# Kernel tuning notes

Hardware: AMD Instinct MI355X
Metric: run time of the kernel (lower is better)

Reference implementation:

```python
import math
import jax, jax.numpy as jnp
import numpy as np


def setup_inputs() -> dict:
    key = jax.random.key(0)
    k0, k1, k2 = jax.random.split(key, 3)
    b, c, h, w = 4, 256, 64, 64
    x = jax.random.normal(k0, (b, c, h, w), dtype=jnp.float32)
    # 1x1 conv weights stored as [out_ch, in_ch]
    qkv_w = jax.random.normal(k1, (3 * c, c), dtype=jnp.float32) / math.sqrt(c)
    qkv_b = jnp.zeros((3 * c,), dtype=jnp.float32)
    out_w = jax.random.normal(k2, (c, c), dtype=jnp.float32) / math.sqrt(c)
    out_b = jnp.zeros((c,), dtype=jnp.float32)
    return {"x": x, "qkv_w": qkv_w, "qkv_b": qkv_b, "out_w": out_w, "out_b": out_b}


def reference(x, qkv_w, qkv_b, out_w, out_b):
    b, c, h, w = x.shape
    n = h * w
    # 1x1 conv QKV projection: [b, 3c, h, w]
    qkv = jnp.einsum('oc,bchw->bohw', qkv_w, x) + qkv_b[None, :, None, None]
    # chunk along channels into q, k, v each [b, c, n]
    qkv = qkv.reshape(b, 3, c, n)
    q, k, v = qkv[:, 0], qkv[:, 1], qkv[:, 2]
    # attn[b, i, j] = sum_c k[b,c,i] * q[b,c,j] / sqrt(c); softmax over key axis (dim=-2 -> axis=1)
    scores = jnp.einsum('bcn,bcm->bnm', k, q) / math.sqrt(c)
    attn = jax.nn.softmax(scores, axis=1)
    # out[b, c, j] = sum_i v[b,c,i] * attn[b,i,j]
    o = jnp.einsum('bcn,bnm->bcm', v, attn).reshape(b, c, h, w)
    # output 1x1 conv
    return jnp.einsum('oc,bchw->bohw', out_w, o) + out_b[None, :, None, None]
```

## Files before the change

kernel.cpp:

```cpp
#include <hip/hip_runtime.h>
#include <hip/hip_bf16.h>

typedef unsigned short u16;
typedef unsigned int u32;
typedef __attribute__((ext_vector_type(8))) short short8;
typedef __attribute__((ext_vector_type(4))) short short4v;
typedef __attribute__((ext_vector_type(16))) float f32x16;
typedef __attribute__((ext_vector_type(4))) float f32x4;

#define MFMA32 __builtin_amdgcn_mfma_f32_32x32x16_bf16
#define MFMA16 __builtin_amdgcn_mfma_f32_16x16x32_bf16

#define NSEQ 4096
#define CD 256
#define CF 0.09016844005556021f

__device__ __forceinline__ u16 f2bf(float f) {
  u32 u = __float_as_uint(f);
  u += 0x7fffu + ((u >> 16) & 1u);
  return (u16)(u >> 16);
}
__device__ __forceinline__ float bf2f(short s) {
  return __uint_as_float(((u32)(u16)s) << 16);
}
__device__ __forceinline__ u32 pk2bf(float a, float b) {
  union {
    __hip_bfloat162 h;
    u32 u;
  } cv;
  cv.h = __float22bfloat162_rn(make_float2(a, b));
  return cv.u;
}
__device__ __forceinline__ void async16(const void* g, void* l) {
  __builtin_amdgcn_global_load_lds(
      (const __attribute__((address_space(1))) u32*)g,
      (__attribute__((address_space(3))) u32*)l, 16, 0, 0);
}

__global__ __launch_bounds__(256) void xpose_cast(const float* __restrict__ x,
                                                  u16* __restrict__ x_t,
                                                  const float* __restrict__ qkv_w,
                                                  const float* __restrict__ out_w,
                                                  u16* __restrict__ wq,
                                                  u16* __restrict__ wo) {
  __shared__ float tile[64][65];
  const int t = threadIdx.x;
  {
    int lin = blockIdx.x + 64 * (blockIdx.y + 4 * blockIdx.z);
    int widx = lin * 256 + t;
    if (widx < 768 * CD)
      wq[widx] = f2bf(qkv_w[widx]);
    else
      wo[widx - 768 * CD] = f2bf(out_w[widx - 768 * CD]);
  }
  const int b = blockIdx.z;
  const int n0 = blockIdx.x * 64, c0 = blockIdx.y * 64;
  const float* xb = x + (size_t)b * CD * NSEQ;
  const int cr = t >> 4, nc4 = (t & 15) * 4;
#pragma unroll
  for (int i = 0; i < 4; ++i) {
    int c = cr + 16 * i;
    float4 v = *(const float4*)(xb + (size_t)(c0 + c) * NSEQ + n0 + nc4);
    tile[c][nc4 + 0] = v.x;
    tile[c][nc4 + 1] = v.y;
    tile[c][nc4 + 2] = v.z;
    tile[c][nc4 + 3] = v.w;
  }
  __syncthreads();
  const int n = t & 63, cc = (t >> 6) * 16;
  u16* dst = x_t + (size_t)b * NSEQ * CD + (size_t)(n0 + n) * CD + c0 + cc;
#pragma unroll
  for (int j = 0; j < 4; ++j) {
    short4v pv;
#pragma unroll
    for (int r = 0; r < 4; ++r) pv[r] = (short)f2bf(tile[cc + 4 * j + r][n]);
    *(short4v*)(dst + 4 * j) = pv;
  }
}

__global__ __launch_bounds__(512, 1) void qkv_gemm3(
    const u16* __restrict__ wq, const float* __restrict__ qkv_b,
    const u16* __restrict__ x_t, u16* __restrict__ q_t, u16* __restrict__ k_t,
    u16* __restrict__ v_) {
  __shared__ u16 __align__(16) Wls[128 * 256];
  __shared__ u16 __align__(16) Bls[128 * 256];
  const int t = threadIdx.x, w = t >> 6, lane = t & 63;
  const int l31 = lane & 31, l5 = lane >> 5;
  const int os = w & 3, nh = w >> 2;
  const int n0 = blockIdx.x * 128, o0 = blockIdx.y * 128, b = blockIdx.z;
  const u16* Xb = x_t + (size_t)b * NSEQ * CD;
#pragma unroll
  for (int j = 0; j < 8; ++j) {
    int r = w * 16 + j * 2 + l5;
    async16(wq + (size_t)(o0 + r) * CD + ((l31 ^ (r & 7)) * 8),
            Wls + (w * 16 + j * 2) * 256);
    async16(Xb + (size_t)(n0 + r) * CD + ((l31 ^ (r & 7)) * 8),
            Bls + (w * 16 + j * 2) * 256);
  }
  __builtin_amdgcn_s_waitcnt(0);
  __syncthreads();
  f32x16 acc0, acc1;
#pragma unroll
  for (int i = 0; i < 16; ++i) {
    acc0[i] = 0.f;
    acc1[i] = 0.f;
  }
  const int ra = os * 32 + l31;
  const int rb0 = nh * 64 + l31, rb1 = rb0 + 32;
#pragma unroll
  for (int kc = 0; kc < 16; ++kc) {
    short8 a = *(const short8*)(Wls + ra * 256 + (((kc * 2 + l5) ^ (ra & 7)) * 8));
    short8 b0 = *(const short8*)(Bls + rb0 * 256 + (((kc * 2 + l5) ^ (rb0 & 7)) * 8));
    short8 b1 = *(const short8*)(Bls + rb1 * 256 + (((kc * 2 + l5) ^ (rb1 & 7)) * 8));
    acc0 = MFMA32(a, b0, acc0, 0, 0, 0);
    acc1 = MFMA32(a, b1, acc1, 0, 0, 0);
  }
  const int otype = blockIdx.y >> 1;
  const int obase = o0 + os * 32;
#pragma unroll
  for (int na = 0; na < 2; ++na) {
    f32x16& acc = na ? acc1 : acc0;
    const int n_g = n0 + nh * 64 + na * 32 + l31;
    if (otype < 2) {
      u16* dst = (otype == 0 ? q_t : k_t) + (size_t)b * NSEQ * CD +
                 (size_t)n_g * CD + (obase - otype * 256);
#pragma unroll
      for (int g = 0; g < 4; ++g) {
        float4 bv = *(const float4*)(qkv_b + obase + g * 8 + l5 * 4);
        const float* bp = (const float*)&bv;
        short4v pk;
#pragma unroll
        for (int r = 0; r < 4; ++r) pk[r] = (short)f2bf(acc[g * 4 + r] + bp[r]);
        *(short4v*)(dst + g * 8 + l5 * 4) = pk;
      }
    } else {
      u16* dst = v_ + (size_t)b * CD * NSEQ;
#pragma unroll
      for (int g = 0; g < 4; ++g) {
        float4 bv = *(const float4*)(qkv_b + obase + g * 8 + l5 * 4);
        const float* bp = (const float*)&bv;
#pragma unroll
        for (int r = 0; r < 4; ++r) {
          int c = obase - 512 + g * 8 + l5 * 4 + r;
          dst[(size_t)c * NSEQ + n_g] = f2bf(acc[g * 4 + r] + bp[r]);
        }
      }
    }
  }
}

__global__ __launch_bounds__(512, 4) void flash9(const u16* __restrict__ q_t,
                                                 const u16* __restrict__ k_t,
                                                 const u16* __restrict__ v_,
                                                 u16* __restrict__ opart,
                                                 float2* __restrict__ ml) {
  __shared__ u16 __align__(16) Kls[2][32 * 256];
  __shared__ u16 __align__(16) Vls[2][128 * 64];

  const int t = threadIdx.x, w = t >> 6, lane = t & 63;
  const int l31 = lane & 31, l5 = lane >> 5;
  const int l15 = lane & 15, g = lane >> 4;

  const int linear = blockIdx.x;
  const int xcd = linear & 7, slot = linear >> 3;
  const int b = xcd >> 1;
  const int q = (xcd & 1) * 2 + (slot >> 5);
  const int mblk = slot & 31;
  const int m0 = mblk * 128;
  const int nbase = q * 1024;

  const u16* Qb = q_t + (size_t)b * NSEQ * CD;
  const u16* Kb = k_t + (size_t)b * NSEQ * CD;
  const u16* Vb = v_ + (size_t)b * CD * NSEQ;

  const int mrow = m0 + w * 16 + l15;

  short8 qf[8];
#pragma unroll
  for (int kk = 0; kk < 8; ++kk)
    qf[kk] = *(const short8*)(Qb + (size_t)mrow * CD + kk * 32 + g * 8);

  const u16* ksrc[2];
#pragma unroll
  for (int j = 0; j < 2; ++j) {
    int kr = w * 4 + j * 2 + l5;
    ksrc[j] = Kb + (size_t)kr * CD + ((l31 ^ (kr & 7)) * 8);
  }
  const u16* vsrc[2];
#pragma unroll
  for (int j = 0; j < 2; ++j) {
    int c2 = w * 16 + j * 8 + (lane >> 3);
    int chl = (lane & 7) ^ (c2 & 7);
    int c = (c2 << 1) | (chl >> 2);
    vsrc[j] = Vb + (size_t)c * NSEQ + (chl & 3) * 8;
  }

#pragma unroll
  for (int j = 0; j < 2; ++j) {
    async16(ksrc[j] + (size_t)nbase * CD, &Kls[0][(w * 4 + j * 2) * 256]);
    async16(vsrc[j] + nbase, &Vls[0][(w * 16 + j * 8) * 64]);
  }

  float mst = -3.0e38f, lst = 0.f;
  f32x4 oa[16];
#pragma unroll
  for (int i = 0; i < 16; ++i)
#pragma unroll
    for (int r = 0; r < 4; ++r) oa[i][r] = 0.f;

  const int vbase =
      (l15 >> 1) * 64 + (((((l15 & 1) << 2) | g) ^ ((l15 >> 1) & 7)) * 8);
  const int kx = l15 & 7;

  for (int tt = 0; tt < 32; ++tt) {
    const int cur = tt & 1;
    __builtin_amdgcn_s_waitcnt(0);
    __syncthreads();
    if (tt + 1 < 32) {
      const int n0 = nbase + (tt + 1) * 32;
      const int nxt = cur ^ 1;
#pragma unroll
      for (int j = 0; j < 2; ++j) {
        async16(ksrc[j] + (size_t)n0 * CD, &Kls[nxt][(w * 4 + j * 2) * 256]);
        async16(vsrc[j] + n0, &Vls[nxt][(w * 16 + j * 8) * 64]);
      }
    }
    f32x4 sa0, sa1;
#pragma unroll
    for (int r = 0; r < 4; ++r) {
      sa0[r] = 0.f;
      sa1[r] = 0.f;
    }
    __builtin_amdgcn_s_setprio(1);
#pragma unroll
    for (int kk = 0; kk < 8; ++kk) {
      const int ch = kk * 4 + g;
      short8 a0 = *(const short8*)(&Kls[cur][l15 * 256 + ((ch ^ kx) * 8)]);
      short8 a1 =
          *(const short8*)(&Kls[cur][(16 + l15) * 256 + ((ch ^ kx) * 8)]);
      sa0 = MFMA16(a0, qf[kk], sa0, 0, 0, 0);
      sa1 = MFMA16(a1, qf[kk], sa1, 0, 0, 0);
    }
    __builtin_amdgcn_s_setprio(0);
    float rm = fmaxf(fmaxf(fmaxf(sa0[0], sa0[1]), fmaxf(sa0[2], sa0[3])),
                     fmaxf(fmaxf(sa1[0], sa1[1]), fmaxf(sa1[2], sa1[3])));
    rm = fmaxf(rm, __shfl_xor(rm, 16));
    rm = fmaxf(rm, __shfl_xor(rm, 32));
    float mnew = fmaxf(mst, rm * CF);
    float al = exp2f(mst - mnew);
    mst = mnew;
    float p00 = exp2f(sa0[0] * CF - mnew), p01 = exp2f(sa0[1] * CF - mnew);
    float p02 = exp2f(sa0[2] * CF - mnew), p03 = exp2f(sa0[3] * CF - mnew);
    float p10 = exp2f(sa1[0] * CF - mnew), p11 = exp2f(sa1[1] * CF - mnew);
    float p12 = exp2f(sa1[2] * CF - mnew), p13 = exp2f(sa1[3] * CF - mnew);
    float ls = ((p00 + p01) + (p02 + p03)) + ((p10 + p11) + (p12 + p13));
    ls += __shfl_xor(ls, 16);
    ls += __shfl_xor(ls, 32);
    lst = lst * al + ls;
    if (__ballot(al != 1.0f)) {
#pragma unroll
      for (int i = 0; i < 16; ++i)
#pragma unroll
        for (int r = 0; r < 4; ++r) oa[i][r] *= al;
    }
    u32 A0 = pk2bf(p00, p01), A1 = pk2bf(p02, p03);
    u32 B0 = pk2bf(p10, p11), B1 = pk2bf(p12, p13);
    const int g0 = g & 1, h = g >> 1;
    u32 ea0 = (u32)__shfl_xor((int)A0, 16), ea1 = (u32)__shfl_xor((int)A1, 16);
    u32 eb0 = (u32)__shfl_xor((int)B0, 16), eb1 = (u32)__shfl_xor((int)B1, 16);
    u32 CA0 = g0 ? ea0 : A0, CA1 = g0 ? ea1 : A1;
    u32 CA2 = g0 ? A0 : ea0, CA3 = g0 ? A1 : ea1;
    u32 CB0 = g0 ? eb0 : B0, CB1 = g0 ? eb1 : B1;
    u32 CB2 = g0 ? B0 : eb0, CB3 = g0 ? B1 : eb1;
    u32 s0 = h ? CA0 : CB0, s1 = h ? CA1 : CB1;
    u32 s2 = h ? CA2 : CB2, s3 = h ? CA3 : CB3;
    u32 r0 = (u32)__shfl_xor((int)s0, 32), r1 = (u32)__shfl_xor((int)s1, 32);
    u32 r2 = (u32)__shfl_xor((int)s2, 32), r3 = (u32)__shfl_xor((int)s3, 32);
    u32 k0 = h ? CB0 : CA0, k1 = h ? CB1 : CA1;
    u32 k2 = h ? CB2 : CA2, k3 = h ? CB3 : CA3;
    const bool own = (g0 == h);
    union {
      u32 u[4];
      short8 s8;
    } pfv;
    pfv.u[0] = own ? k0 : r0;
    pfv.u[1] = own ? k1 : r1;
    pfv.u[2] = own ? k2 : r2;
    pfv.u[3] = own ? k3 : r3;
    short8 pf = pfv.s8;
    __builtin_amdgcn_s_setprio(1);
#pragma unroll
    for (int ct = 0; ct < 16; ++ct) {
      short8 vf = *(const short8*)(&Vls[cur][ct * 512 + vbase]);
      oa[ct] = MFMA16(vf, pf, oa[ct], 0, 0, 0);
    }
    __builtin_amdgcn_s_setprio(0);
  }

  float inv = 1.0f / lst;
  u16* dst = opart + ((size_t)(q * 4 + b) * NSEQ + mrow) * CD;
#pragma unroll
  for (int ct = 0; ct < 16; ++ct) {
    short4v pk;
#pragma unroll
    for (int r = 0; r < 4; ++r) pk[r] = (short)f2bf(oa[ct][r] * inv);
    *(short4v*)(dst + ct * 16 + g * 4) = pk;
  }
  if (lane < 16)
    ml[(size_t)(q * 4 + b) * NSEQ + mrow] = make_float2(mst, lst);
}

__global__ __launch_bounds__(512, 1) void out_gemm6(
    const u16* __restrict__ wo, const float* __restrict__ out_b,
    const u16* __restrict__ opart, const float2* __restrict__ ml,
    float* __restrict__ out) {
  __shared__ u16 __align__(16) Wls[128 * 256];
  __shared__ u16 __align__(16) Bls[128 * 256];
  const int t = threadIdx.x, w = t >> 6, lane = t & 63;
  const int l31 = lane & 31, l5 = lane >> 5;
  const int os = w & 3, nh = w >> 2;
  const int n0 = blockIdx.x * 128, o0 = blockIdx.y * 128, b = blockIdx.z;
#pragma unroll
  for (int j = 0; j < 8; ++j) {
    int r = w * 16 + j * 2 + l5;
    async16(wo + (size_t)(o0 + r) * CD + ((l31 ^ (r & 7)) * 8),
            Wls + (w * 16 + j * 2) * 256);
  }
#pragma unroll
  for (int i = 0; i < 8; ++i) {
    int idx = i * 512 + t;
    int r = idx >> 5, p = idx & 31;
    int n = n0 + r;
    float2 st[4];
#pragma unroll
    for (int qq = 0; qq < 4; ++qq) st[qq] = ml[(size_t)(qq * 4 + b) * NSEQ + n];
    float M = fmaxf(fmaxf(st[0].x, st[1].x), fmaxf(st[2].x, st[3].x));
    float wt[4], tot = 0.f;
#pragma unroll
    for (int qq = 0; qq < 4; ++qq) {
      wt[qq] = st[qq].y * exp2f(st[qq].x - M);
      tot += wt[qq];
    }
    float inv = 1.0f / tot;
    float acc[8] = {};
#pragma unroll
    for (int qq = 0; qq < 4; ++qq) {
      float wq_ = wt[qq] * inv;
      short8 xq =
          *(const short8*)(opart + ((size_t)(qq * 4 + b) * NSEQ + n) * CD + p * 8);
#pragma unroll
      for (int e = 0; e < 8; ++e) acc[e] += wq_ * bf2f(xq[e]);
    }
    short8 om;
#pragma unroll
    for (int e = 0; e < 8; ++e) om[e] = (short)f2bf(acc[e]);
    *(short8*)(Bls + r * 256 + ((p ^ (r & 7)) * 8)) = om;
  }
  __builtin_amdgcn_s_waitcnt(0);
  __syncthreads();
  f32x16 acc0, acc1;
#pragma unroll
  for (int i = 0; i < 16; ++i) {
    acc0[i] = 0.f;
    acc1[i] = 0.f;
  }
  const int ra = os * 32 + l31;
  const int rb0 = nh * 64 + l31, rb1 = rb0 + 32;
#pragma unroll
  for (int kc = 0; kc < 16; ++kc) {
    short8 a = *(const short8*)(Wls + ra * 256 + (((kc * 2 + l5) ^ (ra & 7)) * 8));
    short8 b0 = *(const short8*)(Bls + rb0 * 256 + (((kc * 2 + l5) ^ (rb0 & 7)) * 8));
    short8 b1 = *(const short8*)(Bls + rb1 * 256 + (((kc * 2 + l5) ^ (rb1 & 7)) * 8));
    acc0 = MFMA32(a, b0, acc0, 0, 0, 0);
    acc1 = MFMA32(a, b1, acc1, 0, 0, 0);
  }
  const int obase = o0 + os * 32;
#pragma unroll
  for (int na = 0; na < 2; ++na) {
    f32x16& acc = na ? acc1 : acc0;
    const int n_g = n0 + nh * 64 + na * 32 + l31;
#pragma unroll
    for (int g = 0; g < 4; ++g) {
      float4 bv = *(const float4*)(out_b + obase + g * 8 + l5 * 4);
      const float* bp = (const float*)&bv;
#pragma unroll
      for (int r = 0; r < 4; ++r) {
        int o = obase + g * 8 + l5 * 4 + r;
        out[((size_t)b * CD + o) * NSEQ + n_g] = acc[g * 4 + r] + bp[r];
      }
    }
  }
}

extern "C" void kernel_launch(void* const* d_in, const int* in_sizes, int n_in,
                              void* d_out, int out_size, void* d_ws,
                              size_t ws_size, hipStream_t stream) {
  const float* x = (const float*)d_in[0];
  const float* qkv_w = (const float*)d_in[1];
  const float* qkv_b = (const float*)d_in[2];
  const float* out_w = (const float*)d_in[3];
  const float* out_b = (const float*)d_in[4];
  float* out = (float*)d_out;

  const size_t SZ = (size_t)4 * NSEQ * CD;
  u16* x_t = (u16*)d_ws;
  u16* q_t = x_t + SZ;
  u16* k_t = q_t + SZ;
  u16* v_ = k_t + SZ;
  u16* opart = v_ + SZ;
  u16* wq = opart + 4 * SZ;
  u16* wo = wq + 768 * CD;
  float2* ml = (float2*)(wo + CD * CD);

  xpose_cast<<<dim3(64, 4, 4), dim3(256), 0, stream>>>(x, x_t, qkv_w, out_w,
                                                       wq, wo);
  qkv_gemm3<<<dim3(32, 6, 4), dim3(512), 0, stream>>>(wq, qkv_b, x_t, q_t, k_t,
                                                      v_);
  flash9<<<dim3(512), dim3(512), 0, stream>>>(q_t, k_t, v_, opart, ml);
  out_gemm6<<<dim3(32, 2, 4), dim3(512), 0, stream>>>(wo, out_b, opart, ml,
                                                      out);
}
```

Measured before the change: 223.9 us.

## Load V fragments directly from global memory and shrink flash blocks to 4 waves

The flash-attention kernel no longer stages V tiles in shared memory. Each lane now loads its V fragments straight from global memory into registers, software-pipelined across the PV MFMA loop. Blocks shrink from 8 to 4 waves (64 query rows) and the grid doubles, and each wave now issues more K async loads. The aim is to cut LDS traffic and footprint so more blocks fit per CU. The cost is uncoalesced, repeated global V reads per wave and higher register pressure.

```diff
diff --git a/kernel.cpp b/kernel.cpp
--- a/kernel.cpp
+++ b/kernel.cpp
@@ -149,13 +149,12 @@
   }
 }
 
-__global__ __launch_bounds__(512, 4) void flash9(const u16* __restrict__ q_t,
-                                                 const u16* __restrict__ k_t,
-                                                 const u16* __restrict__ v_,
-                                                 u16* __restrict__ opart,
-                                                 float2* __restrict__ ml) {
+__global__ __launch_bounds__(256, 3) void flash10(const u16* __restrict__ q_t,
+                                                  const u16* __restrict__ k_t,
+                                                  const u16* __restrict__ v_,
+                                                  u16* __restrict__ opart,
+                                                  float2* __restrict__ ml) {
   __shared__ u16 __align__(16) Kls[2][32 * 256];
-  __shared__ u16 __align__(16) Vls[2][128 * 64];
 
   const int t = threadIdx.x, w = t >> 6, lane = t & 63;
   const int l31 = lane & 31, l5 = lane >> 5;
@@ -164,9 +163,9 @@
   const int linear = blockIdx.x;
   const int xcd = linear & 7, slot = linear >> 3;
   const int b = xcd >> 1;
-  const int q = (xcd & 1) * 2 + (slot >> 5);
-  const int mblk = slot & 31;
-  const int m0 = mblk * 128;
+  const int q = (xcd & 1) * 2 + (slot >> 6);
+  const int mblk = slot & 63;
+  const int m0 = mblk * 64;
   const int nbase = q * 1024;
 
   const u16* Qb = q_t + (size_t)b * NSEQ * CD;
@@ -180,26 +179,16 @@
   for (int kk = 0; kk < 8; ++kk)
     qf[kk] = *(const short8*)(Qb + (size_t)mrow * CD + kk * 32 + g * 8);
 
-  const u16* ksrc[2];
-#pragma unroll
-  for (int j = 0; j < 2; ++j) {
-    int kr = w * 4 + j * 2 + l5;
+  const u16* ksrc[4];
+#pragma unroll
+  for (int j = 0; j < 4; ++j) {
+    int kr = w * 8 + j * 2 + l5;
     ksrc[j] = Kb + (size_t)kr * CD + ((l31 ^ (kr & 7)) * 8);
   }
-  const u16* vsrc[2];
-#pragma unroll
-  for (int j = 0; j < 2; ++j) {
-    int c2 = w * 16 + j * 8 + (lane >> 3);
-    int chl = (lane & 7) ^ (c2 & 7);
-    int c = (c2 << 1) | (chl >> 2);
-    vsrc[j] = Vb + (size_t)c * NSEQ + (chl & 3) * 8;
-  }
-
-#pragma unroll
-  for (int j = 0; j < 2; ++j) {
-    async16(ksrc[j] + (size_t)nbase * CD, &Kls[0][(w * 4 + j * 2) * 256]);
-    async16(vsrc[j] + nbase, &Vls[0][(w * 16 + j * 8) * 64]);
-  }
+
+#pragma unroll
+  for (int j = 0; j < 4; ++j)
+    async16(ksrc[j] + (size_t)nbase * CD, &Kls[0][(w * 8 + j * 2) * 256]);
 
   float mst = -3.0e38f, lst = 0.f;
   f32x4 oa[16];
@@ -208,9 +197,8 @@
 #pragma unroll
     for (int r = 0; r < 4; ++r) oa[i][r] = 0.f;
 
-  const int vbase =
-      (l15 >> 1) * 64 + (((((l15 & 1) << 2) | g) ^ ((l15 >> 1) & 7)) * 8);
   const int kx = l15 & 7;
+  const u16* vlane = Vb + (size_t)l15 * NSEQ + nbase + g * 8;
 
   for (int tt = 0; tt < 32; ++tt) {
     const int cur = tt & 1;
@@ -220,10 +208,8 @@
       const int n0 = nbase + (tt + 1) * 32;
       const int nxt = cur ^ 1;
 #pragma unroll
-      for (int j = 0; j < 2; ++j) {
-        async16(ksrc[j] + (size_t)n0 * CD, &Kls[nxt][(w * 4 + j * 2) * 256]);
-        async16(vsrc[j] + n0, &Vls[nxt][(w * 16 + j * 8) * 64]);
-      }
+      for (int j = 0; j < 4; ++j)
+        async16(ksrc[j] + (size_t)n0 * CD, &Kls[nxt][(w * 8 + j * 2) * 256]);
     }
     f32x4 sa0, sa1;
 #pragma unroll
@@ -257,6 +243,11 @@
     ls += __shfl_xor(ls, 16);
     ls += __shfl_xor(ls, 32);
     lst = lst * al + ls;
+    const u16* vt = vlane + tt * 32;
+    short8 vr[8];
+#pragma unroll
+    for (int i = 0; i < 8; ++i)
+      vr[i] = *(const short8*)(vt + (size_t)i * 16 * NSEQ);
     if (__ballot(al != 1.0f)) {
 #pragma unroll
       for (int i = 0; i < 16; ++i)
@@ -291,8 +282,9 @@
     __builtin_amdgcn_s_setprio(1);
 #pragma unroll
     for (int ct = 0; ct < 16; ++ct) {
-      short8 vf = *(const short8*)(&Vls[cur][ct * 512 + vbase]);
-      oa[ct] = MFMA16(vf, pf, oa[ct], 0, 0, 0);
+      short8 cv = vr[ct & 7];
+      if (ct < 8) vr[ct & 7] = *(const short8*)(vt + (size_t)(ct + 8) * 16 * NSEQ);
+      oa[ct] = MFMA16(cv, pf, oa[ct], 0, 0, 0);
     }
     __builtin_amdgcn_s_setprio(0);
   }
@@ -416,7 +408,7 @@
                                                        wq, wo);
   qkv_gemm3<<<dim3(32, 6, 4), dim3(512), 0, stream>>>(wq, qkv_b, x_t, q_t, k_t,
                                                       v_);
-  flash9<<<dim3(512), dim3(512), 0, stream>>>(q_t, k_t, v_, opart, ml);
+  flash10<<<dim3(1024), dim3(256), 0, stream>>>(q_t, k_t, v_, opart, ml);
   out_gemm6<<<dim3(32, 2, 4), dim3(512), 0, stream>>>(wo, out_b, opart, ml,
                                                       out);
 }
```

New measurement: 433.9 us. +93.8%, slower.
